# Performance work log

Measured on AMD Instinct MI355X. Metric: run time of the kernel, lower is better.

The kernel has to match this reference:

```python
import jax, jax.numpy as jnp
import numpy as np

# Model constants (match init_kwargs and fla GatedLinearAttention defaults used in source)
L = 4            # num_layers
D = 1024         # d_model
H = 4            # n_heads
DK = 128         # head key dim  = 0.5*D / H
DV = 256         # head value dim = 1.0*D / H
KD = H * DK      # total key dim = 512
VD = H * DV      # total value dim = 1024
V = 32000        # vocab
B, T = 1, 2048
LR = 16          # gate_low_rank_dim
GLN = 16.0       # gate_logit_normalizer
EPS = 1e-5
SCALE = DK ** -0.5


def setup_inputs() -> dict:
    key = jax.random.key(0)
    ks = jax.random.split(key, 12)
    s = 0.02
    return {
        "input_ids": jax.random.randint(ks[0], (B, T), 0, V),
        "emb": jax.random.normal(ks[1], (V, D), jnp.float32) * s,
        "Wq": jax.random.normal(ks[2], (L, D, KD), jnp.float32) * s,
        "Wk": jax.random.normal(ks[3], (L, D, KD), jnp.float32) * s,
        "Wv": jax.random.normal(ks[4], (L, D, VD), jnp.float32) * s,
        "Wg": jax.random.normal(ks[5], (L, D, VD), jnp.float32) * s,
        "Wgk1": jax.random.normal(ks[6], (L, D, LR), jnp.float32) * s,
        "Wgk2": jax.random.normal(ks[7], (L, LR, KD), jnp.float32) * s,
        "bgk": jnp.zeros((L, KD), jnp.float32),
        "gnw": jnp.ones((L, DV), jnp.float32),
        "Wo": jax.random.normal(ks[8], (L, VD, D), jnp.float32) * s,
        "ln_w": jnp.ones((D,), jnp.float32),
        "ln_b": jnp.zeros((D,), jnp.float32),
        "Wlm": jax.random.normal(ks[9], (D, V), jnp.float32) * s,
        "blm": jnp.zeros((V,), jnp.float32),
    }


def _gla_layer(x, wq, wk, wv, wg, wg1, wg2, bg, nw, wo):
    # x: [B, T, D]
    b, t, _ = x.shape
    q = (x @ wq).reshape(b, t, H, DK) * SCALE
    k = (x @ wk).reshape(b, t, H, DK)
    v = (x @ wv).reshape(b, t, H, DV)
    g = (x @ wg).reshape(b, t, H, DV)
    # low-rank forget gate, log-space, normalized
    gk = (jax.nn.log_sigmoid((x @ wg1) @ wg2 + bg) / GLN).reshape(b, t, H, DK)

    # time-major for scan: [T, B, H, *]
    qt, kt, vt, gkt = (jnp.moveaxis(a, 1, 0) for a in (q, k, v, gk))

    def step(S, inp):
        q_t, k_t, v_t, gk_t = inp  # [B,H,DK], [B,H,DK], [B,H,DV], [B,H,DK]
        S = S * jnp.exp(gk_t)[..., None] + k_t[..., None] * v_t[..., None, :]
        o_t = jnp.einsum('bhk,bhkv->bhv', q_t, S)
        return S, o_t

    S0 = jnp.zeros((b, H, DK, DV), x.dtype)
    _, o = jax.lax.scan(step, S0, (qt, kt, vt, gkt))
    o = jnp.moveaxis(o, 0, 1)  # [B, T, H, DV]
    # fused RMSNorm + swish output gate
    o = o * jax.lax.rsqrt(jnp.mean(o * o, axis=-1, keepdims=True) + EPS) * nw
    o = o * (g * jax.nn.sigmoid(g))
    return o.reshape(b, t, VD) @ wo


def reference(input_ids, emb, Wq, Wk, Wv, Wg, Wgk1, Wgk2, bgk, gnw, Wo, ln_w, ln_b, Wlm, blm):
    h = emb[input_ids]  # [B, T, D]
    for i in range(L):
        h = _gla_layer(h, Wq[i], Wk[i], Wv[i], Wg[i], Wgk1[i], Wgk2[i], bgk[i], gnw[i], Wo[i])
    mu = jnp.mean(h, axis=-1, keepdims=True)
    var = jnp.mean((h - mu) ** 2, axis=-1, keepdims=True)
    h = (h - mu) * jax.lax.rsqrt(var + EPS) * ln_w + ln_b
    return h @ Wlm + blm
```

## Files before the change

kernel.cpp:

```cpp
#include <hip/hip_runtime.h>
#include <hip/hip_bf16.h>
#include <math.h>

#define NL 4
#define TT 2048
#define DD 1024
#define KDIM 512
#define VDIM 1024
#define QSTR 3072
#define NH 4
#define DKH 128
#define DVH 256
#define CH 64
#define NCH 32
#define VOCAB 32000
#define SCALE_Q 0.08838834764831845f

typedef short bf16x8 __attribute__((ext_vector_type(8)));
typedef float f32x4 __attribute__((ext_vector_type(4)));

__device__ __forceinline__ void gload_lds16(const void* g, void* l) {
    __builtin_amdgcn_global_load_lds((const __attribute__((address_space(1))) void*)g,
                                     (__attribute__((address_space(3))) void*)l, 16, 0, 0);
}

__device__ __forceinline__ void store_bf16x4(__hip_bfloat16* p, float a, float b, float c, float d) {
    union { __hip_bfloat16 h[4]; ushort4 v; } r;
    r.h[0] = __float2bfloat16(a); r.h[1] = __float2bfloat16(b);
    r.h[2] = __float2bfloat16(c); r.h[3] = __float2bfloat16(d);
    *(ushort4*)p = r.v;
}

__global__ __launch_bounds__(256) void embed_kernel(const int* __restrict__ ids,
                                                    const float* __restrict__ emb,
                                                    float* __restrict__ h,
                                                    __hip_bfloat16* __restrict__ hb) {
    int idx = blockIdx.x * 256 + threadIdx.x;
    int t = idx >> 8, c4 = idx & 255;
    float4 v = *(const float4*)(emb + (size_t)ids[t] * DD + c4 * 4);
    *(float4*)(h + (size_t)t * DD + c4 * 4) = v;
    store_bf16x4(hb + (size_t)t * DD + c4 * 4, v.x, v.y, v.z, v.w);
}

__global__ __launch_bounds__(256) void tconv_kernel(const float* __restrict__ in,
                                                    __hip_bfloat16* __restrict__ out,
                                                    int K, int N) {
    __shared__ float tle[64][65];
    const int n0 = blockIdx.x * 64, k0 = blockIdx.y * 64;
    const int tid = threadIdx.x;
    const int ty = tid >> 4, tx = tid & 15;
#pragma unroll
    for (int u = 0; u < 4; u++) {
        int r = ty + u * 16;
        float4 v = *(const float4*)(in + (size_t)(k0 + r) * N + n0 + tx * 4);
        tle[r][tx * 4 + 0] = v.x; tle[r][tx * 4 + 1] = v.y;
        tle[r][tx * 4 + 2] = v.z; tle[r][tx * 4 + 3] = v.w;
    }
    __syncthreads();
#pragma unroll
    for (int u = 0; u < 4; u++) {
        int nn = u * 16 + ty;
        store_bf16x4(out + (size_t)(n0 + nn) * K + k0 + tx * 4,
                     tle[tx * 4 + 0][nn], tle[tx * 4 + 1][nn],
                     tle[tx * 4 + 2][nn], tle[tx * 4 + 3][nn]);
    }
}

__global__ __launch_bounds__(256) void tconv_layer_kernel(const float* __restrict__ wq,
                                                          const float* __restrict__ wk,
                                                          const float* __restrict__ wv,
                                                          const float* __restrict__ wg,
                                                          const float* __restrict__ wo,
                                                          __hip_bfloat16* __restrict__ Wt,
                                                          __hip_bfloat16* __restrict__ WoT) {
    __shared__ float tle[64][65];
    int b = blockIdx.x;
    const float* src; __hip_bfloat16* dst; int N, local;
    if (b < 128)      { src = wq; dst = Wt;                         N = 512;  local = b; }
    else if (b < 256) { src = wk; dst = Wt + (size_t)512 * 1024;    N = 512;  local = b - 128; }
    else if (b < 512) { src = wv; dst = Wt + (size_t)1024 * 1024;   N = 1024; local = b - 256; }
    else if (b < 768) { src = wg; dst = Wt + (size_t)2048 * 1024;   N = 1024; local = b - 512; }
    else              { src = wo; dst = WoT;                        N = 1024; local = b - 768; }
    int nbx = N >> 6;
    int n0 = (local % nbx) * 64, k0 = (local / nbx) * 64;
    const int tid = threadIdx.x;
    const int ty = tid >> 4, tx = tid & 15;
#pragma unroll
    for (int u = 0; u < 4; u++) {
        int r = ty + u * 16;
        float4 v = *(const float4*)(src + (size_t)(k0 + r) * N + n0 + tx * 4);
        tle[r][tx * 4 + 0] = v.x; tle[r][tx * 4 + 1] = v.y;
        tle[r][tx * 4 + 2] = v.z; tle[r][tx * 4 + 3] = v.w;
    }
    __syncthreads();
#pragma unroll
    for (int u = 0; u < 4; u++) {
        int nn = u * 16 + ty;
        store_bf16x4(dst + (size_t)(n0 + nn) * 1024 + k0 + tx * 4,
                     tle[tx * 4 + 0][nn], tle[tx * 4 + 1][nn],
                     tle[tx * 4 + 2][nn], tle[tx * 4 + 3][nn]);
    }
}

template<int NF>
__global__ __launch_bounds__(256) void gemm_bf16_db(const __hip_bfloat16* __restrict__ A,
                                                    const __hip_bfloat16* __restrict__ Bt,
                                                    const float* __restrict__ bias,
                                                    float* __restrict__ C,
                                                    __hip_bfloat16* __restrict__ Cb,
                                                    int M, int N, int K) {
    __shared__ short a_lds[2][128 * 32];
    __shared__ short b_lds[2][NF * 32 * 32];
    const int tid = threadIdx.x;
    const int wv = tid >> 6, lane = tid & 63;
    const int wr = wv >> 1, wc = wv & 1;
    const int nbx = gridDim.x;
    int wg = blockIdx.y * nbx + blockIdx.x;
    int cpx = (nbx * gridDim.y) >> 3;
    int swz = (wg & 7) * cpx + (wg >> 3);
    const int m0 = (swz % nbx) * 128, n0 = (swz / nbx) * (NF * 32);
    const int lr = lane & 15, lk = (lane >> 4) * 8;

    f32x4 acc[4][NF];
#pragma unroll
    for (int m = 0; m < 4; m++)
#pragma unroll
        for (int n = 0; n < NF; n++) acc[m][n] = (f32x4)(0.f);

    auto STAGE = [&](int buf, int k0) {
#pragma unroll
        for (int u = 0; u < 2; u++) {
            int s = wv * 128 + u * 64 + lane;
            int r = s >> 2, kc = (s & 3) * 8;
            gload_lds16(A + (size_t)(m0 + r) * K + k0 + kc,
                        &a_lds[buf][(wv * 128 + u * 64) * 8]);
        }
        if constexpr (NF == 4) {
#pragma unroll
            for (int u = 0; u < 2; u++) {
                int s = wv * 128 + u * 64 + lane;
                int r = s >> 2, kc = (s & 3) * 8;
                gload_lds16(Bt + (size_t)(n0 + r) * K + k0 + kc,
                            &b_lds[buf][(wv * 128 + u * 64) * 8]);
            }
        } else {
            int s = wv * 64 + lane;
            int r = s >> 2, kc = (s & 3) * 8;
            gload_lds16(Bt + (size_t)(n0 + r) * K + k0 + kc,
                        &b_lds[buf][(wv * 64) * 8]);
        }
    };
    auto COMPUTE = [&](int buf) {
        bf16x8 af[4], bfr[NF];
#pragma unroll
        for (int m = 0; m < 4; m++)
            af[m] = *(const bf16x8*)&a_lds[buf][(wr * 64 + m * 16 + lr) * 32 + lk];
#pragma unroll
        for (int n = 0; n < NF; n++)
            bfr[n] = *(const bf16x8*)&b_lds[buf][(wc * (NF * 16) + n * 16 + lr) * 32 + lk];
#pragma unroll
        for (int m = 0; m < 4; m++)
#pragma unroll
            for (int n = 0; n < NF; n++)
                acc[m][n] = __builtin_amdgcn_mfma_f32_16x16x32_bf16(af[m], bfr[n], acc[m][n], 0, 0, 0);
    };

    STAGE(0, 0);
    __syncthreads();
    int cur = 0;
    for (int k0 = 32; k0 < K; k0 += 32) {
        STAGE(cur ^ 1, k0);
        COMPUTE(cur);
        __syncthreads();
        cur ^= 1;
    }
    COMPUTE(cur);

    const int rbase = (lane >> 4) * 4;
#pragma unroll
    for (int n = 0; n < NF; n++) {
        int col = n0 + wc * (NF * 16) + n * 16 + lr;
        float bv = bias ? bias[col] : 0.f;
#pragma unroll
        for (int m = 0; m < 4; m++) {
            int row = m0 + wr * 64 + m * 16 + rbase;
#pragma unroll
            for (int r = 0; r < 4; r++) {
                float val = acc[m][n][r] + bv;
                C[(size_t)(row + r) * N + col] = val;
                if (Cb) Cb[(size_t)(row + r) * N + col] = __float2bfloat16(val);
            }
        }
    }
}

__device__ __forceinline__ void lm_stage(const __hip_bfloat16* src, int row0,
                                         char* dst, int kt32, int wv, int lane, int K) {
#pragma unroll
    for (int ii = 0; ii < 2; ii++) {
        int o = (wv * 2 + ii) * 1024;
        int ob = o + lane * 16;
        int lg = ob ^ (((ob >> 7) & 7) << 4);
        int row = lg >> 6;
        int ce = (lg & 63) >> 1;
        gload_lds16(src + (size_t)(row0 + row) * K + kt32 * 32 + ce, dst + o);
    }
}

__device__ __forceinline__ bf16x8 lm_frag(const char* sub, int row, int lk2) {
    int lg = ((row >> 1) << 7) + ((row & 1) << 6) + lk2;
    return *(const bf16x8*)(sub + (lg ^ (((row >> 1) & 7) << 4)));
}

template<int PT, bool LOADB, int VM>
__device__ __forceinline__ void lm_phase(const char* aT, const char* bT,
                                         const __hip_bfloat16* ssrc, int srow0,
                                         char* sdst, int skt32,
                                         bf16x8 (&bfr)[4][2], f32x4 (&acc)[8][4],
                                         int wr, int wc, int lr, int lk2,
                                         int wv, int lane, int K) {
    if constexpr (LOADB) {
#pragma unroll
        for (int n = 0; n < 4; n++)
#pragma unroll
            for (int ks = 0; ks < 2; ks++)
                bfr[n][ks] = lm_frag(bT + ks * 16384, wc * 64 + n * 16 + lr, lk2);
    }
    bf16x8 af[2][2];
#pragma unroll
    for (int mm = 0; mm < 2; mm++)
#pragma unroll
        for (int ks = 0; ks < 2; ks++)
            af[mm][ks] = lm_frag(aT + ks * 16384, wr * 128 + (2 * PT + mm) * 16 + lr, lk2);
    lm_stage(ssrc, srow0, sdst, skt32, wv, lane, K);
    asm volatile("s_barrier" ::: "memory");
    __builtin_amdgcn_s_setprio(1);
#pragma unroll
    for (int mm = 0; mm < 2; mm++)
#pragma unroll
        for (int n = 0; n < 4; n++) {
            acc[2 * PT + mm][n] = __builtin_amdgcn_mfma_f32_16x16x32_bf16(af[mm][0], bfr[n][0], acc[2 * PT + mm][n], 0, 0, 0);
            acc[2 * PT + mm][n] = __builtin_amdgcn_mfma_f32_16x16x32_bf16(af[mm][1], bfr[n][1], acc[2 * PT + mm][n], 0, 0, 0);
        }
    __builtin_amdgcn_s_setprio(0);
    if constexpr (VM == 2) asm volatile("s_waitcnt vmcnt(2)" ::: "memory");
    asm volatile("s_barrier" ::: "memory");
}

__global__ __launch_bounds__(512, 1) void gemm256_lm(const __hip_bfloat16* __restrict__ A,
                                                     const __hip_bfloat16* __restrict__ Bt,
                                                     const float* __restrict__ bias,
                                                     float* __restrict__ C,
                                                     int M, int N, int K) {
    extern __shared__ __align__(16) char smem[];
    char* sA0 = smem;
    char* sA1 = smem + 32768;
    char* sB0 = smem + 65536;
    char* sB1 = smem + 98304;
    const int tid = threadIdx.x;
    const int wv = tid >> 6, lane = tid & 63;
    const int wr = wv >> 2, wc = wv & 3;
    const int lr = lane & 15, lk2 = (lane >> 4) * 16;

    const int nbx = gridDim.x;
    int wg = blockIdx.y * nbx + blockIdx.x;
    int cpx = (nbx * gridDim.y) >> 3;
    int swz = (wg & 7) * cpx + (wg >> 3);
    const int m0 = (swz % nbx) * 256;
    const int n0 = (swz / nbx) * 256;

    f32x4 acc[8][4];
#pragma unroll
    for (int m = 0; m < 8; m++)
#pragma unroll
        for (int n = 0; n < 4; n++) acc[m][n] = (f32x4)(0.f);

    const int NTI = K / 64;
    const int NI  = NTI / 2;

    lm_stage(A,  m0, sA0 + 0,     0, wv, lane, K);
    lm_stage(A,  m0, sA0 + 16384, 1, wv, lane, K);
    lm_stage(Bt, n0, sB0 + 0,     0, wv, lane, K);
    lm_stage(Bt, n0, sB0 + 16384, 1, wv, lane, K);
    lm_stage(Bt, n0, sB1 + 0,     2, wv, lane, K);
    lm_stage(Bt, n0, sB1 + 16384, 3, wv, lane, K);
    asm volatile("s_waitcnt vmcnt(0)" ::: "memory");
    asm volatile("s_barrier" ::: "memory");

    for (int i = 0; i < NI; i++) {
        int tOdd = 2 * i + 1;
        int tE   = 2 * i + 2 < NTI ? 2 * i + 2 : NTI - 1;
        int tB3  = 2 * i + 3 < NTI ? 2 * i + 3 : NTI - 1;
        bf16x8 bfr[4][2];
        lm_phase<0, true , 0>(sA0, sB0, A,  m0, sA1 + 0,     2 * tOdd + 0, bfr, acc, wr, wc, lr, lk2, wv, lane, K);
        lm_phase<1, false, 0>(sA0, sB0, A,  m0, sA1 + 16384, 2 * tOdd + 1, bfr, acc, wr, wc, lr, lk2, wv, lane, K);
        lm_phase<2, false, 0>(sA0, sB0, Bt, n0, sB0 + 0,     2 * tE   + 0, bfr, acc, wr, wc, lr, lk2, wv, lane, K);
        lm_phase<3, false, 2>(sA0, sB0, Bt, n0, sB0 + 16384, 2 * tE   + 1, bfr, acc, wr, wc, lr, lk2, wv, lane, K);
        lm_phase<0, true , 0>(sA1, sB1, A,  m0, sA0 + 0,     2 * tE   + 0, bfr, acc, wr, wc, lr, lk2, wv, lane, K);
        lm_phase<1, false, 0>(sA1, sB1, A,  m0, sA0 + 16384, 2 * tE   + 1, bfr, acc, wr, wc, lr, lk2, wv, lane, K);
        lm_phase<2, false, 0>(sA1, sB1, Bt, n0, sB1 + 0,     2 * tB3  + 0, bfr, acc, wr, wc, lr, lk2, wv, lane, K);
        lm_phase<3, false, 2>(sA1, sB1, Bt, n0, sB1 + 16384, 2 * tB3  + 1, bfr, acc, wr, wc, lr, lk2, wv, lane, K);
    }

    const int r4 = (lane >> 4) * 4;
#pragma unroll
    for (int n = 0; n < 4; n++) {
        int col = n0 + wc * 64 + n * 16 + lr;
        float bv = bias ? bias[col] : 0.f;
#pragma unroll
        for (int m = 0; m < 8; m++) {
            int row = m0 + wr * 128 + m * 16 + r4;
#pragma unroll
            for (int r = 0; r < 4; r++)
                C[(size_t)(row + r) * N + col] = acc[m][n][r] + bv;
        }
    }
}

__global__ __launch_bounds__(256) void lowrank1_kernel(const float* __restrict__ h,
                                                       const float* __restrict__ W1,
                                                       float* __restrict__ xg) {
    int t = blockIdx.x;
    int tid = threadIdx.x;
    int j = tid & 15, ks = tid >> 4;
    const float* hr = h + (size_t)t * DD + ks * 64;
    const float* w = W1 + (size_t)(ks * 64) * 16 + j;
    float acc = 0.f;
#pragma unroll 8
    for (int kk = 0; kk < 64; kk++) acc = fmaf(hr[kk], w[kk * 16], acc);
    __shared__ float red[16][17];
    red[ks][j] = acc;
    __syncthreads();
    if (tid < 16) {
        float s = 0.f;
#pragma unroll
        for (int r = 0; r < 16; r++) s += red[r][tid];
        xg[t * 16 + tid] = s;
    }
}

__global__ __launch_bounds__(256) void gatefuse2_kernel(const float* __restrict__ qkvg,
                                                        const float* __restrict__ xg,
                                                        const float* __restrict__ W2,
                                                        const float* __restrict__ bg,
                                                        float* __restrict__ Gl,
                                                        __hip_bfloat16* __restrict__ qhB,
                                                        __hip_bfloat16* __restrict__ khB,
                                                        __hip_bfloat16* __restrict__ ktT) {
    __shared__ float w2s[16][64];
    __shared__ float xgs[64][16];
    __shared__ float part[4][64];
    const int tid = threadIdx.x;
    const int j = tid & 63, sg = tid >> 6;
    const int cg = blockIdx.x & 7, c = blockIdx.x >> 3;
    const int col = cg * 64 + j;
#pragma unroll
    for (int r = 0; r < 4; r++)
        w2s[sg * 4 + r][j] = W2[(size_t)(sg * 4 + r) * KDIM + col];
#pragma unroll
    for (int u = 0; u < 4; u++) {
        int id = u * 256 + tid;
        int t = id >> 4, r = id & 15;
        xgs[t][r] = xg[(size_t)(c * 64 + t) * 16 + r];
    }
    __syncthreads();
    const float bgv = bg[col];
    float ls[16];
    float partial = 0.f;
#pragma unroll
    for (int i = 0; i < 16; i++) {
        int t = sg * 16 + i;
        float s = bgv;
#pragma unroll
        for (int r = 0; r < 16; r++) s = fmaf(xgs[t][r], w2s[r][j], s);
        float v = (fminf(s, 0.f) - log1pf(expf(-fabsf(s)))) * (1.f / 16.f);
        ls[i] = v;
        partial += v;
    }
    part[sg][j] = partial;
    __syncthreads();
    float base = 0.f, total = 0.f;
#pragma unroll
    for (int r = 0; r < 4; r++) {
        float p = part[r][j];
        if (r < sg) base += p;
        total += p;
    }
    if (sg == 0) Gl[c * KDIM + col] = total;
    const float eGl = expf(total);
    const int hh = col >> 7, dk = col & 127;
    __hip_bfloat16 ktbuf[16];
    float G = base;
#pragma unroll
    for (int i = 0; i < 16; i++) {
        int t = c * 64 + sg * 16 + i;
        G += ls[i];
        const float* qp = qkvg + (size_t)t * QSTR + col;
        float qv = qp[0], kv = qp[512];
        qhB[(size_t)t * KDIM + col] = __float2bfloat16(qv * expf(G) * SCALE_Q);
        float khv = kv * expf(-G);
        khB[(size_t)t * KDIM + col] = __float2bfloat16(khv);
        ktbuf[i] = __float2bfloat16(khv * eGl);
    }
    __hip_bfloat16* kp = ktT + ((size_t)(c * NH + hh) * DKH + dk) * CH + sg * 16;
    *(uint4*)(kp + 0) = *(uint4*)&ktbuf[0];
    *(uint4*)(kp + 8) = *(uint4*)&ktbuf[8];
}

__global__ __launch_bounds__(256) void vtrans_kernel(const float* __restrict__ qkvg,
                                                     __hip_bfloat16* __restrict__ vT) {
    __shared__ float tle[64][65];
    int bid = blockIdx.x;
    int dvq = bid & 3, hh = (bid >> 2) & 3, c = bid >> 4;
    int tid = threadIdx.x, ty = tid >> 4, tx = tid & 15;
#pragma unroll
    for (int u = 0; u < 4; u++) {
        int r = u * 16 + ty;
        float4 v = *(const float4*)(qkvg + (size_t)(c * 64 + r) * QSTR + 1024 + hh * DVH + dvq * 64 + tx * 4);
        tle[r][tx * 4 + 0] = v.x; tle[r][tx * 4 + 1] = v.y;
        tle[r][tx * 4 + 2] = v.z; tle[r][tx * 4 + 3] = v.w;
    }
    __syncthreads();
    __hip_bfloat16* dst = vT + ((size_t)(c * NH + hh) * DVH + dvq * 64) * CH;
#pragma unroll
    for (int u = 0; u < 4; u++) {
        int dv = u * 16 + ty;
        store_bf16x4(dst + (size_t)dv * CH + tx * 4,
                     tle[tx * 4 + 0][dv], tle[tx * 4 + 1][dv],
                     tle[tx * 4 + 2][dv], tle[tx * 4 + 3][dv]);
    }
}

__global__ __launch_bounds__(256) void chunkU_mfma(const __hip_bfloat16* __restrict__ vT,
                                                   const __hip_bfloat16* __restrict__ ktT,
                                                   __hip_bfloat16* __restrict__ U) {
    const int ch = blockIdx.x;
    const __hip_bfloat16* Ap = vT + (size_t)ch * DVH * CH;
    const __hip_bfloat16* Bp = ktT + (size_t)ch * DKH * CH;
    __hip_bfloat16* Cp = U + (size_t)ch * DVH * DKH;
    const int tid = threadIdx.x, wv = tid >> 6, lane = tid & 63;
    const int wr = wv >> 1, wc = wv & 1;
    const int lr = lane & 15, lk = (lane >> 4) * 8;
    f32x4 acc[8][4];
#pragma unroll
    for (int m = 0; m < 8; m++)
#pragma unroll
        for (int n = 0; n < 4; n++) acc[m][n] = (f32x4)(0.f);
#pragma unroll
    for (int ks = 0; ks < 2; ks++) {
        bf16x8 a[8], b[4];
#pragma unroll
        for (int m = 0; m < 8; m++)
            a[m] = *(const bf16x8*)(Ap + (size_t)(wr * 128 + m * 16 + lr) * CH + ks * 32 + lk);
#pragma unroll
        for (int n = 0; n < 4; n++)
            b[n] = *(const bf16x8*)(Bp + (size_t)(wc * 64 + n * 16 + lr) * CH + ks * 32 + lk);
#pragma unroll
        for (int m = 0; m < 8; m++)
#pragma unroll
            for (int n = 0; n < 4; n++)
                acc[m][n] = __builtin_amdgcn_mfma_f32_16x16x32_bf16(a[m], b[n], acc[m][n], 0, 0, 0);
    }
    const int r4 = (lane >> 4) * 4;
#pragma unroll
    for (int m = 0; m < 8; m++)
#pragma unroll
        for (int n = 0; n < 4; n++)
#pragma unroll
            for (int r = 0; r < 4; r++)
                Cp[(size_t)(wr * 128 + m * 16 + r4 + r) * DKH + wc * 64 + n * 16 + lr] =
                    __float2bfloat16(acc[m][n][r]);
}

__global__ __launch_bounds__(256) void scan_states_kernel(__hip_bfloat16* __restrict__ U,
                                                          const float* __restrict__ Gl) {
    int idx = blockIdx.x * 256 + threadIdx.x;
    int hh = idx >> 15, dv = (idx >> 7) & 255, dk = idx & 127;
    int col = hh * DKH + dk;
    float s = 0.f;
    for (int c = 0; c < NCH; c++) {
        __hip_bfloat16* p = U + ((size_t)(c * NH + hh) * DVH + dv) * DKH + dk;
        float u = __bfloat162float(*p);
        *p = __float2bfloat16(s);
        s = s * expf(Gl[c * KDIM + col]) + u;
    }
}

__global__ __launch_bounds__(256) void attn_rms_mfma(const __hip_bfloat16* __restrict__ qhB,
                                                     const __hip_bfloat16* __restrict__ khB,
                                                     const __hip_bfloat16* __restrict__ vT,
                                                     const __hip_bfloat16* __restrict__ Ub,
                                                     const float* __restrict__ qkvg,
                                                     const float* __restrict__ nw,
                                                     __hip_bfloat16* __restrict__ obb) {
    __shared__ __hip_bfloat16 P[32 * 72];
    __shared__ float sums[32][2];
    const int bid = blockIdx.x;
    const int rh = bid & 1, hh = (bid >> 1) & 3, c = bid >> 3;
    const int t0 = c * CH;
    const int tid = threadIdx.x, wv = tid >> 6, lane = tid & 63;
    const int half = wv >> 1, rg = wv & 1;
    const int lr = lane & 15, lk = (lane >> 4) * 8;
    const int r4 = (lane >> 4) * 4;
    const int rr = rh * 32 + rg * 16;

    bf16x8 qf[4];
#pragma unroll
    for (int ks = 0; ks < 4; ks++)
        qf[ks] = *(const bf16x8*)(qhB + (size_t)(t0 + rr + lr) * KDIM + hh * DKH + ks * 32 + lk);

    if (half == 0) {
        f32x4 s[4];
#pragma unroll
        for (int n = 0; n < 4; n++) s[n] = (f32x4)(0.f);
#pragma unroll
        for (int n = 0; n < 4; n++)
#pragma unroll
            for (int ks = 0; ks < 4; ks++) {
                bf16x8 kf = *(const bf16x8*)(khB + (size_t)(t0 + n * 16 + lr) * KDIM + hh * DKH + ks * 32 + lk);
                s[n] = __builtin_amdgcn_mfma_f32_16x16x32_bf16(qf[ks], kf, s[n], 0, 0, 0);
            }
#pragma unroll
        for (int n = 0; n < 4; n++)
#pragma unroll
            for (int r = 0; r < 4; r++) {
                int i = rr + r4 + r, j = n * 16 + lr;
                float val = (j <= i) ? s[n][r] : 0.f;
                P[(rg * 16 + r4 + r) * 72 + j] = __float2bfloat16(val);
            }
    }
    __syncthreads();

    const __hip_bfloat16* vTp = vT + ((size_t)(c * NH + hh) * DVH + half * 128) * CH;
    const __hip_bfloat16* Ubp = Ub + ((size_t)(c * NH + hh) * DVH + half * 128) * DKH;
    bf16x8 pf[2];
#pragma unroll
    for (int ks = 0; ks < 2; ks++)
        pf[ks] = *(const bf16x8*)&P[(rg * 16 + lr) * 72 + ks * 32 + lk];

    f32x4 o[8];
#pragma unroll
    for (int n = 0; n < 8; n++) o[n] = (f32x4)(0.f);
#pragma unroll
    for (int n = 0; n < 8; n++) {
#pragma unroll
        for (int ks = 0; ks < 2; ks++) {
            bf16x8 vf = *(const bf16x8*)(vTp + (size_t)(n * 16 + lr) * CH + ks * 32 + lk);
            o[n] = __builtin_amdgcn_mfma_f32_16x16x32_bf16(pf[ks], vf, o[n], 0, 0, 0);
        }
#pragma unroll
        for (int ks = 0; ks < 4; ks++) {
            bf16x8 uf = *(const bf16x8*)(Ubp + (size_t)(n * 16 + lr) * DKH + ks * 32 + lk);
            o[n] = __builtin_amdgcn_mfma_f32_16x16x32_bf16(qf[ks], uf, o[n], 0, 0, 0);
        }
    }

    float part[4];
#pragma unroll
    for (int r = 0; r < 4; r++) {
        float p = 0.f;
#pragma unroll
        for (int n = 0; n < 8; n++) p = fmaf(o[n][r], o[n][r], p);
        part[r] = p;
    }
#pragma unroll
    for (int off = 1; off < 16; off <<= 1)
#pragma unroll
        for (int r = 0; r < 4; r++) part[r] += __shfl_xor(part[r], off);
    if (lr == 0)
#pragma unroll
        for (int r = 0; r < 4; r++) sums[rg * 16 + r4 + r][half] = part[r];
    __syncthreads();

#pragma unroll
    for (int r = 0; r < 4; r++) {
        int lrow = rg * 16 + r4 + r;
        int t = t0 + rh * 32 + lrow;
        float tot = sums[lrow][0] + sums[lrow][1];
        float rinv = rsqrtf(tot * (1.f / 256.f) + 1e-5f);
#pragma unroll
        for (int n = 0; n < 8; n++) {
            int col = half * 128 + n * 16 + lr;
            float gv = qkvg[(size_t)t * QSTR + 2048 + hh * DVH + col];
            float val = o[n][r] * rinv * nw[col] * (gv / (1.f + expf(-gv)));
            obb[(size_t)t * VDIM + hh * DVH + col] = __float2bfloat16(val);
        }
    }
}

__global__ __launch_bounds__(256) void ln_kernel(const float* __restrict__ h,
                                                 const float* __restrict__ w,
                                                 const float* __restrict__ b,
                                                 __hip_bfloat16* __restrict__ out16) {
    int t = blockIdx.x;
    int tid = threadIdx.x;
    float4 x = *(const float4*)(h + (size_t)t * DD + tid * 4);
    float s = x.x + x.y + x.z + x.w;
    float ss = x.x * x.x + x.y * x.y + x.z * x.z + x.w * x.w;
#pragma unroll
    for (int off = 32; off > 0; off >>= 1) {
        s += __shfl_xor(s, off);
        ss += __shfl_xor(ss, off);
    }
    __shared__ float rs[4], rss[4];
    int wv = tid >> 6;
    if ((tid & 63) == 0) { rs[wv] = s; rss[wv] = ss; }
    __syncthreads();
    s = rs[0] + rs[1] + rs[2] + rs[3];
    ss = rss[0] + rss[1] + rss[2] + rss[3];
    float mu = s * (1.f / 1024.f);
    float var = ss * (1.f / 1024.f) - mu * mu;
    float r = rsqrtf(var + 1e-5f);
    float4 wv4 = *(const float4*)(w + tid * 4);
    float4 bv4 = *(const float4*)(b + tid * 4);
    store_bf16x4(out16 + (size_t)t * DD + tid * 4,
                 (x.x - mu) * r * wv4.x + bv4.x,
                 (x.y - mu) * r * wv4.y + bv4.y,
                 (x.z - mu) * r * wv4.z + bv4.z,
                 (x.w - mu) * r * wv4.w + bv4.w);
}

extern "C" void kernel_launch(void* const* d_in, const int* in_sizes, int n_in,
                              void* d_out, int out_size, void* d_ws, size_t ws_size,
                              hipStream_t stream) {
    const int*   ids  = (const int*)d_in[0];
    const float* emb  = (const float*)d_in[1];
    const float* Wq   = (const float*)d_in[2];
    const float* Wk   = (const float*)d_in[3];
    const float* Wv   = (const float*)d_in[4];
    const float* Wg   = (const float*)d_in[5];
    const float* Wgk1 = (const float*)d_in[6];
    const float* Wgk2 = (const float*)d_in[7];
    const float* bgk  = (const float*)d_in[8];
    const float* gnw  = (const float*)d_in[9];
    const float* Wo   = (const float*)d_in[10];
    const float* lnw  = (const float*)d_in[11];
    const float* lnb  = (const float*)d_in[12];
    const float* Wlm  = (const float*)d_in[13];
    const float* blm  = (const float*)d_in[14];
    float* out = (float*)d_out;

    float* ws = (float*)d_ws;
    float* h    = ws; ws += (size_t)TT * DD;
    float* qkvg = ws; ws += (size_t)TT * QSTR;
    float* xg   = ws; ws += (size_t)TT * 16;
    float* Gl   = ws; ws += (size_t)NCH * KDIM;
    __hip_bfloat16* hb    = (__hip_bfloat16*)ws; ws += (size_t)TT * DD / 2;
    __hip_bfloat16* obb   = (__hip_bfloat16*)ws; ws += (size_t)TT * DD / 2;
    __hip_bfloat16* lnb16 = (__hip_bfloat16*)ws; ws += (size_t)TT * DD / 2;
    __hip_bfloat16* qhB   = (__hip_bfloat16*)ws; ws += (size_t)TT * KDIM / 2;
    __hip_bfloat16* khB   = (__hip_bfloat16*)ws; ws += (size_t)TT * KDIM / 2;
    __hip_bfloat16* ktT   = (__hip_bfloat16*)ws; ws += (size_t)NCH * NH * DKH * CH / 2;
    __hip_bfloat16* vT    = (__hip_bfloat16*)ws; ws += (size_t)NCH * NH * DVH * CH / 2;
    __hip_bfloat16* Ub    = (__hip_bfloat16*)ws; ws += (size_t)NCH * NH * DVH * DKH / 2;
    __hip_bfloat16* Wt    = (__hip_bfloat16*)ws; ws += (size_t)QSTR * DD / 2;
    __hip_bfloat16* WoT   = (__hip_bfloat16*)ws; ws += (size_t)VDIM * DD / 2;
    __hip_bfloat16* WlmT  = (__hip_bfloat16*)ws; ws += (size_t)VOCAB * DD / 2;

    hipFuncSetAttribute((const void*)gemm256_lm,
                        hipFuncAttributeMaxDynamicSharedMemorySize, 131072);

    embed_kernel<<<TT, 256, 0, stream>>>(ids, emb, h, hb);
    tconv_kernel<<<dim3(VOCAB / 64, DD / 64), 256, 0, stream>>>(Wlm, WlmT, DD, VOCAB);

    for (int l = 0; l < NL; l++) {
        const float* w1 = Wgk1 + (size_t)l * DD * 16;
        const float* w2 = Wgk2 + (size_t)l * 16 * KDIM;
        const float* bg = bgk + (size_t)l * KDIM;
        const float* nw = gnw + (size_t)l * DVH;

        tconv_layer_kernel<<<1024, 256, 0, stream>>>(Wq + (size_t)l * DD * KDIM,
                                                     Wk + (size_t)l * DD * KDIM,
                                                     Wv + (size_t)l * DD * VDIM,
                                                     Wg + (size_t)l * DD * VDIM,
                                                     Wo + (size_t)l * VDIM * DD, Wt, WoT);
        gemm_bf16_db<4><<<dim3(TT / 128, QSTR / 128), 256, 0, stream>>>(hb, Wt, nullptr, qkvg, nullptr, TT, QSTR, DD);
        lowrank1_kernel<<<TT, 256, 0, stream>>>(h, w1, xg);
        gatefuse2_kernel<<<NCH * (KDIM / 64), 256, 0, stream>>>(qkvg, xg, w2, bg, Gl, qhB, khB, ktT);
        vtrans_kernel<<<NCH * NH * 4, 256, 0, stream>>>(qkvg, vT);
        chunkU_mfma<<<NCH * NH, 256, 0, stream>>>(vT, ktT, Ub);
        scan_states_kernel<<<NH * DVH * DKH / 256, 256, 0, stream>>>(Ub, Gl);
        attn_rms_mfma<<<NCH * NH * 2, 256, 0, stream>>>(qhB, khB, vT, Ub, qkvg, nw, obb);
        gemm_bf16_db<2><<<dim3(TT / 128, DD / 64), 256, 0, stream>>>(obb, WoT, nullptr, h, hb, TT, DD, VDIM);
    }

    ln_kernel<<<TT, 256, 0, stream>>>(h, lnw, lnb, lnb16);
    gemm256_lm<<<dim3(TT / 256, VOCAB / 256), 512, 131072, stream>>>(lnb16, WlmT, blm, out, TT, VOCAB, DD);
}
```

Baseline: 660.6 us.

## Batch per-layer weight transposes, deepen LM-head load pipeline, use nontemporal output stores

The four per-layer weight transpose/convert launches become one kernel that converts all layers up front into per-layer bf16 buffers. This cuts launch count and gives the conversion a larger grid, at the cost of more workspace. The LM-head GEMM now waits with vmcnt(4) instead of vmcnt(2), keeping more global-to-LDS loads in flight. The fp32 logits are written with nontemporal stores so the large output does not pollute the cache.

```diff
diff --git a/kernel.cpp b/kernel.cpp
--- a/kernel.cpp
+++ b/kernel.cpp
@@ -66,15 +66,23 @@
     }
 }
 
-__global__ __launch_bounds__(256) void tconv_layer_kernel(const float* __restrict__ wq,
-                                                          const float* __restrict__ wk,
-                                                          const float* __restrict__ wv,
-                                                          const float* __restrict__ wg,
-                                                          const float* __restrict__ wo,
-                                                          __hip_bfloat16* __restrict__ Wt,
-                                                          __hip_bfloat16* __restrict__ WoT) {
+__global__ __launch_bounds__(256) void tconv_all_kernel(const float* __restrict__ Wq,
+                                                        const float* __restrict__ Wk,
+                                                        const float* __restrict__ Wv,
+                                                        const float* __restrict__ Wg,
+                                                        const float* __restrict__ Wo,
+                                                        __hip_bfloat16* __restrict__ Wt4,
+                                                        __hip_bfloat16* __restrict__ WoT4) {
     __shared__ float tle[64][65];
-    int b = blockIdx.x;
+    int l = blockIdx.x >> 10;
+    int b = blockIdx.x & 1023;
+    const float* wq = Wq + (size_t)l * DD * KDIM;
+    const float* wk = Wk + (size_t)l * DD * KDIM;
+    const float* wv = Wv + (size_t)l * DD * VDIM;
+    const float* wg = Wg + (size_t)l * DD * VDIM;
+    const float* wo = Wo + (size_t)l * VDIM * DD;
+    __hip_bfloat16* Wt  = Wt4  + (size_t)l * QSTR * DD;
+    __hip_bfloat16* WoT = WoT4 + (size_t)l * DD * VDIM;
     const float* src; __hip_bfloat16* dst; int N, local;
     if (b < 128)      { src = wq; dst = Wt;                         N = 512;  local = b; }
     else if (b < 256) { src = wk; dst = Wt + (size_t)512 * 1024;    N = 512;  local = b - 128; }
@@ -243,7 +251,7 @@
             acc[2 * PT + mm][n] = __builtin_amdgcn_mfma_f32_16x16x32_bf16(af[mm][1], bfr[n][1], acc[2 * PT + mm][n], 0, 0, 0);
         }
     __builtin_amdgcn_s_setprio(0);
-    if constexpr (VM == 2) asm volatile("s_waitcnt vmcnt(2)" ::: "memory");
+    if constexpr (VM == 4) asm volatile("s_waitcnt vmcnt(4)" ::: "memory");
     asm volatile("s_barrier" ::: "memory");
 }
 
@@ -295,11 +303,11 @@
         lm_phase<0, true , 0>(sA0, sB0, A,  m0, sA1 + 0,     2 * tOdd + 0, bfr, acc, wr, wc, lr, lk2, wv, lane, K);
         lm_phase<1, false, 0>(sA0, sB0, A,  m0, sA1 + 16384, 2 * tOdd + 1, bfr, acc, wr, wc, lr, lk2, wv, lane, K);
         lm_phase<2, false, 0>(sA0, sB0, Bt, n0, sB0 + 0,     2 * tE   + 0, bfr, acc, wr, wc, lr, lk2, wv, lane, K);
-        lm_phase<3, false, 2>(sA0, sB0, Bt, n0, sB0 + 16384, 2 * tE   + 1, bfr, acc, wr, wc, lr, lk2, wv, lane, K);
+        lm_phase<3, false, 4>(sA0, sB0, Bt, n0, sB0 + 16384, 2 * tE   + 1, bfr, acc, wr, wc, lr, lk2, wv, lane, K);
         lm_phase<0, true , 0>(sA1, sB1, A,  m0, sA0 + 0,     2 * tE   + 0, bfr, acc, wr, wc, lr, lk2, wv, lane, K);
         lm_phase<1, false, 0>(sA1, sB1, A,  m0, sA0 + 16384, 2 * tE   + 1, bfr, acc, wr, wc, lr, lk2, wv, lane, K);
         lm_phase<2, false, 0>(sA1, sB1, Bt, n0, sB1 + 0,     2 * tB3  + 0, bfr, acc, wr, wc, lr, lk2, wv, lane, K);
-        lm_phase<3, false, 2>(sA1, sB1, Bt, n0, sB1 + 16384, 2 * tB3  + 1, bfr, acc, wr, wc, lr, lk2, wv, lane, K);
+        lm_phase<3, false, 4>(sA1, sB1, Bt, n0, sB1 + 16384, 2 * tB3  + 1, bfr, acc, wr, wc, lr, lk2, wv, lane, K);
     }
 
     const int r4 = (lane >> 4) * 4;
@@ -312,7 +320,8 @@
             int row = m0 + wr * 128 + m * 16 + r4;
 #pragma unroll
             for (int r = 0; r < 4; r++)
-                C[(size_t)(row + r) * N + col] = acc[m][n][r] + bv;
+                __builtin_nontemporal_store(acc[m][n][r] + bv,
+                                            C + (size_t)(row + r) * N + col);
         }
     }
 }
@@ -653,14 +662,15 @@
     __hip_bfloat16* ktT   = (__hip_bfloat16*)ws; ws += (size_t)NCH * NH * DKH * CH / 2;
     __hip_bfloat16* vT    = (__hip_bfloat16*)ws; ws += (size_t)NCH * NH * DVH * CH / 2;
     __hip_bfloat16* Ub    = (__hip_bfloat16*)ws; ws += (size_t)NCH * NH * DVH * DKH / 2;
-    __hip_bfloat16* Wt    = (__hip_bfloat16*)ws; ws += (size_t)QSTR * DD / 2;
-    __hip_bfloat16* WoT   = (__hip_bfloat16*)ws; ws += (size_t)VDIM * DD / 2;
+    __hip_bfloat16* Wt4   = (__hip_bfloat16*)ws; ws += (size_t)NL * QSTR * DD / 2;
+    __hip_bfloat16* WoT4  = (__hip_bfloat16*)ws; ws += (size_t)NL * DD * VDIM / 2;
     __hip_bfloat16* WlmT  = (__hip_bfloat16*)ws; ws += (size_t)VOCAB * DD / 2;
 
     hipFuncSetAttribute((const void*)gemm256_lm,
                         hipFuncAttributeMaxDynamicSharedMemorySize, 131072);
 
     embed_kernel<<<TT, 256, 0, stream>>>(ids, emb, h, hb);
+    tconv_all_kernel<<<NL * 1024, 256, 0, stream>>>(Wq, Wk, Wv, Wg, Wo, Wt4, WoT4);
     tconv_kernel<<<dim3(VOCAB / 64, DD / 64), 256, 0, stream>>>(Wlm, WlmT, DD, VOCAB);
 
     for (int l = 0; l < NL; l++) {
@@ -668,12 +678,9 @@
         const float* w2 = Wgk2 + (size_t)l * 16 * KDIM;
         const float* bg = bgk + (size_t)l * KDIM;
         const float* nw = gnw + (size_t)l * DVH;
-
-        tconv_layer_kernel<<<1024, 256, 0, stream>>>(Wq + (size_t)l * DD * KDIM,
-                                                     Wk + (size_t)l * DD * KDIM,
-                                                     Wv + (size_t)l * DD * VDIM,
-                                                     Wg + (size_t)l * DD * VDIM,
-                                                     Wo + (size_t)l * VDIM * DD, Wt, WoT);
+        const __hip_bfloat16* Wt  = Wt4  + (size_t)l * QSTR * DD;
+        const __hip_bfloat16* WoT = WoT4 + (size_t)l * DD * VDIM;
+
         gemm_bf16_db<4><<<dim3(TT / 128, QSTR / 128), 256, 0, stream>>>(hb, Wt, nullptr, qkvg, nullptr, TT, QSTR, DD);
         lowrank1_kernel<<<TT, 256, 0, stream>>>(h, w1, xg);
         gatefuse2_kernel<<<NCH * (KDIM / 64), 256, 0, stream>>>(qkvg, xg, w2, bg, Gl, qhB, khB, ktT);
```

Result: no change. 648.9 us (-1.8%).
